# Performance work log

Hardware: AMD Instinct MI355X
Metric: run time of the kernel (lower is better)

## Reference

```python
import jax, jax.numpy as jnp
import numpy as np

N_HEADS = 16
EPS = 1e-5


def layer_norm(x, g, b):
    mu = jnp.mean(x, axis=-1, keepdims=True)
    var = jnp.mean(jnp.square(x - mu), axis=-1, keepdims=True)
    return (x - mu) * jax.lax.rsqrt(var + EPS) * g + b


def mhsa(X, wq, wk, wv, wfc, bfc):
    S, D = X.shape
    dk = D // N_HEADS
    scale = 1.0 / np.sqrt(dk).astype(np.float32)
    Q = (X @ wq).reshape(S, N_HEADS, dk).transpose(1, 0, 2)  # (H,S,dk)
    K = (X @ wk).reshape(S, N_HEADS, dk).transpose(1, 0, 2)
    V = (X @ wv).reshape(S, N_HEADS, dk).transpose(1, 0, 2)
    scores = jnp.einsum('hsd,htd->hst', Q, K) * scale
    attn = jax.nn.softmax(scores, axis=-1)
    ctx = jnp.einsum('hst,htd->hsd', attn, V)  # (H,S,dk)
    # Faithful to original torch code: transpose(1,2) on (H,S,dk) -> (H,dk,S),
    # then reshape(-1, H*dk). This scrambles features but is the module's math.
    ctx = jnp.transpose(ctx, (0, 2, 1)).reshape(-1, N_HEADS * dk)  # (S, H*dk)
    return ctx @ wfc + bfc


def setup_inputs() -> dict:
    key = jax.random.key(0)
    S, D = 2048, 2048
    ks = jax.random.split(key, 16)
    sd = 0.02
    p = lambda k, shp: jax.random.normal(k, shp, dtype=jnp.float32) * sd
    return {
        'X': jax.random.normal(ks[0], (S, D), dtype=jnp.float32),
        'wq1': p(ks[1], (D, D)), 'wk1': p(ks[2], (D, D)), 'wv1': p(ks[3], (D, D)),
        'wfc1': p(ks[4], (D, D)), 'bfc1': jnp.zeros((D,), jnp.float32),
        'g1': jnp.ones((D,), jnp.float32), 'b1': jnp.zeros((D,), jnp.float32),
        'wl1': p(ks[5], (D, D)), 'bl1': jnp.zeros((D,), jnp.float32),
        'g2': jnp.ones((D,), jnp.float32), 'b2': jnp.zeros((D,), jnp.float32),
        'wq2': p(ks[6], (D, D)), 'wk2': p(ks[7], (D, D)), 'wv2': p(ks[8], (D, D)),
        'wfc2': p(ks[9], (D, D)), 'bfc2': jnp.zeros((D,), jnp.float32),
        'g3': jnp.ones((D,), jnp.float32), 'b3': jnp.zeros((D,), jnp.float32),
        'wl2': p(ks[10], (D, D)), 'bl2': jnp.zeros((D,), jnp.float32),
        'g4': jnp.ones((D,), jnp.float32), 'b4': jnp.zeros((D,), jnp.float32),
    }


def reference(X, wq1, wk1, wv1, wfc1, bfc1, g1, b1, wl1, bl1, g2, b2,
              wq2, wk2, wv2, wfc2, bfc2, g3, b3, wl2, bl2, g4, b4):
    out = mhsa(X, wq1, wk1, wv1, wfc1, bfc1)
    X = layer_norm(out + X, g1, b1)
    out = X @ wl1 + bl1
    X = layer_norm(out + X, g2, b2)
    out = mhsa(X, wq2, wk2, wv2, wfc2, bfc2)
    X = layer_norm(out + X, g3, b3)
    out = X @ wl2 + bl2
    X = layer_norm(out + X, g4, b4)
    return X
```

## Files before the change

kernel.cpp:

```cpp
#include <hip/hip_runtime.h>
#include <stdint.h>

typedef __bf16 bf16_t;
typedef __bf16 bf16x8 __attribute__((ext_vector_type(8)));
typedef float  f32x4  __attribute__((ext_vector_type(4)));
typedef unsigned short u16x4 __attribute__((ext_vector_type(4)));

__device__ __forceinline__ void gl_lds16(const void* g, void* lds) {
  __builtin_amdgcn_global_load_lds(
      (const __attribute__((address_space(1))) uint32_t*)g,
      (__attribute__((address_space(3))) uint32_t*)lds, 16, 0, 0);
}

template<bool OUT_BF16, bool HAS_BIAS, bool HAS_RES>
__global__ __launch_bounds__(256)
void gemm_bt(const bf16_t* __restrict__ A, int64_t lda, int64_t sA,
             const bf16_t* __restrict__ BT, int64_t ldb, int64_t sB,
             void* __restrict__ Cv, int64_t ldc, int64_t sC,
             const float* __restrict__ bias, const float* __restrict__ res,
             float scale, int K)
{
  __shared__ __align__(16) bf16_t lA[128 * 32];
  __shared__ __align__(16) bf16_t lB[128 * 32];
  const int t = threadIdx.x;
  const int z = blockIdx.z;

  const int gx  = gridDim.x;
  const int nwg = gx * gridDim.y;
  int flat = blockIdx.y * gx + blockIdx.x;
  if ((nwg & 7) == 0) flat = (flat & 7) * (nwg >> 3) + (flat >> 3);
  const int tn = flat % gx;
  const int tm = flat / gx;

  const bf16_t* Ab = A + (int64_t)z * sA;
  const bf16_t* Bb = BT + (int64_t)z * sB;
  const int64_t bm = (int64_t)tm * 128;
  const int64_t bn = (int64_t)tn * 128;
  const int l   = t & 63;
  const int wid = t >> 6;
  const int wm  = (wid >> 1) * 64;
  const int wn  = (wid & 1) * 64;
  const int lr  = l & 15;
  const int kg  = l >> 4;
  const int srow = t >> 2;
  const int scol = (t & 3) * 8;
  char* lAc = (char*)lA;
  char* lBc = (char*)lB;
  const int wbase = (t & 192) * 16;

  f32x4 acc[4][4] = {};

  for (int k0 = 0; k0 < K; k0 += 32) {
    const bf16_t* ga = Ab + (bm + srow) * lda + k0 + scol;
    const bf16_t* gb = Bb + (bn + srow) * ldb + k0 + scol;
    gl_lds16(ga,            lAc + wbase);
    gl_lds16(ga + 64 * lda, lAc + 4096 + wbase);
    gl_lds16(gb,            lBc + wbase);
    gl_lds16(gb + 64 * ldb, lBc + 4096 + wbase);
    __syncthreads();
    bf16x8 af[4], bfv[4];
#pragma unroll
    for (int m = 0; m < 4; ++m)
      af[m] = *(const bf16x8*)(lA + (wm + m * 16 + lr) * 32 + kg * 8);
#pragma unroll
    for (int n = 0; n < 4; ++n)
      bfv[n] = *(const bf16x8*)(lB + (wn + n * 16 + lr) * 32 + kg * 8);
#pragma unroll
    for (int m = 0; m < 4; ++m)
#pragma unroll
      for (int n = 0; n < 4; ++n)
        acc[m][n] = __builtin_amdgcn_mfma_f32_16x16x32_bf16(af[m], bfv[n], acc[m][n], 0, 0, 0);
    __syncthreads();
  }

  bf16_t* C16 = (bf16_t*)Cv + (int64_t)z * sC;
  float*  C32 = (float*)Cv + (int64_t)z * sC;
#pragma unroll
  for (int m = 0; m < 4; ++m) {
#pragma unroll
    for (int n = 0; n < 4; ++n) {
      const int64_t col = bn + wn + n * 16 + lr;
      const float bv = HAS_BIAS ? bias[col] : 0.0f;
#pragma unroll
      for (int r = 0; r < 4; ++r) {
        const int64_t row = bm + wm + m * 16 + kg * 4 + r;
        float v = acc[m][n][r] * scale + bv;
        if constexpr (HAS_RES) v += res[row * ldc + col];
        if constexpr (OUT_BF16) C16[row * ldc + col] = (bf16_t)v;
        else                    C32[row * ldc + col] = v;
      }
    }
  }
}

__global__ __launch_bounds__(256)
void flash_attn(const bf16_t* __restrict__ QKV,
                const bf16_t* __restrict__ VT,
                bf16_t* __restrict__ CTXT)
{
  __shared__ __align__(16) bf16_t lK[64 * 128];
  __shared__ __align__(16) bf16_t lV[128 * 64];
  __shared__ __align__(16) bf16_t lP[4][16 * 64];
  const int t = threadIdx.x;
  const int w = t >> 6, l = t & 63, lo = l & 15, hi = l >> 4;
  const int head = blockIdx.y;
  const int qt = blockIdx.x;
  const int q0 = qt * 64 + w * 16;
  const int wbase = (t & 192) * 16;

  const bf16_t* qp = QKV + (int64_t)(q0 + lo) * 6144 + head * 128 + hi * 8;
  bf16x8 qf[4];
#pragma unroll
  for (int kk = 0; kk < 4; ++kk) qf[kk] = *(const bf16x8*)(qp + 32 * kk);

  const bf16_t* kbase = QKV + 2048 + head * 128;
  const bf16_t* vbase = VT + (int64_t)(head * 128) * 2048;

  float m_r[4], l_r[4];
  f32x4 Oacc[8] = {};
#pragma unroll
  for (int r = 0; r < 4; ++r) { m_r[r] = -3.0e38f; l_r[r] = 0.f; }

  const float c1 = 0.08838834764831845f * 1.4426950408889634f;

  char* lKc = (char*)lK;
  char* lVc = (char*)lV;
  char* pw  = (char*)lP[w];

  for (int tile = 0; tile < 32; ++tile) {
    const int kv0 = tile * 64;
#pragma unroll
    for (int c = 0; c < 4; ++c) {
      const int row = c * 16 + (t >> 4);
      const int srcb = ((t & 15) * 16) ^ ((row & 7) << 4);
      gl_lds16(kbase + (int64_t)(kv0 + row) * 6144 + (srcb >> 1), lKc + c * 4096 + wbase);
    }
#pragma unroll
    for (int c = 0; c < 4; ++c) {
      const int row = c * 32 + (t >> 3);
      const int srcb = ((t & 7) * 16) ^ ((row & 7) << 4);
      gl_lds16(vbase + (int64_t)row * 2048 + kv0 + (srcb >> 1), lVc + c * 4096 + wbase);
    }
    __syncthreads();

    f32x4 Sacc[4] = {};
#pragma unroll
    for (int kk = 0; kk < 4; ++kk) {
      bf16x8 kb[4];
#pragma unroll
      for (int n = 0; n < 4; ++n) {
        const int row = n * 16 + lo;
        kb[n] = *(const bf16x8*)(lKc + row * 256 + ((kk * 64 + hi * 16) ^ ((row & 7) << 4)));
      }
#pragma unroll
      for (int n = 0; n < 4; ++n)
        Sacc[n] = __builtin_amdgcn_mfma_f32_16x16x32_bf16(qf[kk], kb[n], Sacc[n], 0, 0, 0);
    }

    float corr[4];
#pragma unroll
    for (int r = 0; r < 4; ++r) {
      float mx = Sacc[0][r];
#pragma unroll
      for (int n = 1; n < 4; ++n) mx = fmaxf(mx, Sacc[n][r]);
#pragma unroll
      for (int off = 1; off < 16; off <<= 1) mx = fmaxf(mx, __shfl_xor(mx, off));
      const float mt = mx * c1;
      const float mnew = fmaxf(m_r[r], mt);
      corr[r] = exp2f(m_r[r] - mnew);
      m_r[r] = mnew;
    }
    float psum[4] = {0.f, 0.f, 0.f, 0.f};
#pragma unroll
    for (int n = 0; n < 4; ++n) {
#pragma unroll
      for (int r = 0; r < 4; ++r) {
        const float p = exp2f(Sacc[n][r] * c1 - m_r[r]);
        psum[r] += p;
        const int row = hi * 4 + r;
        const int byte = row * 128 + (((n * 16 + lo) * 2) ^ ((row & 7) << 4));
        *(bf16_t*)(pw + byte) = (bf16_t)p;
      }
    }
#pragma unroll
    for (int r = 0; r < 4; ++r) {
#pragma unroll
      for (int off = 1; off < 16; off <<= 1) psum[r] += __shfl_xor(psum[r], off);
      l_r[r] = l_r[r] * corr[r] + psum[r];
    }
#pragma unroll
    for (int n = 0; n < 8; ++n) {
      Oacc[n][0] *= corr[0]; Oacc[n][1] *= corr[1];
      Oacc[n][2] *= corr[2]; Oacc[n][3] *= corr[3];
    }
    asm volatile("s_waitcnt lgkmcnt(0)" ::: "memory");
    __builtin_amdgcn_sched_barrier(0);

#pragma unroll
    for (int kk = 0; kk < 2; ++kk) {
      const bf16x8 pa = *(const bf16x8*)(pw + lo * 128 + ((kk * 64 + hi * 16) ^ ((lo & 7) << 4)));
#pragma unroll
      for (int n = 0; n < 8; ++n) {
        const int row = n * 16 + lo;
        const bf16x8 vb = *(const bf16x8*)(lVc + row * 128 + ((kk * 64 + hi * 16) ^ ((row & 7) << 4)));
        Oacc[n] = __builtin_amdgcn_mfma_f32_16x16x32_bf16(pa, vb, Oacc[n], 0, 0, 0);
      }
    }
    __syncthreads();
  }

  float inv[4];
#pragma unroll
  for (int r = 0; r < 4; ++r) inv[r] = 1.0f / l_r[r];
#pragma unroll
  for (int n = 0; n < 8; ++n) {
    u16x4 o;
#pragma unroll
    for (int r = 0; r < 4; ++r) {
      const bf16_t b = (bf16_t)(Oacc[n][r] * inv[r]);
      o[r] = *(const unsigned short*)&b;
    }
    *(u16x4*)(CTXT + (int64_t)(head * 128 + n * 16 + lo) * 2048 + q0 + hi * 4) = o;
  }
}

template<typename TIN>
__device__ __forceinline__
void transpose_body(const TIN* __restrict__ in, int64_t ldi,
                    bf16_t* __restrict__ out, int64_t ldo)
{
  __shared__ float tile[32][33];
  const int bx = blockIdx.x * 32;
  const int by = blockIdx.y * 32;
  const int tx = threadIdx.x & 31;
  const int ty = threadIdx.x >> 5;
#pragma unroll
  for (int i = 0; i < 32; i += 8)
    tile[ty + i][tx] = (float)in[(int64_t)(by + ty + i) * ldi + bx + tx];
  __syncthreads();
#pragma unroll
  for (int i = 0; i < 32; i += 8)
    out[(int64_t)(bx + ty + i) * ldo + by + tx] = (bf16_t)tile[tx][ty + i];
}

template<typename TIN>
__global__ __launch_bounds__(256)
void transpose_to_bf16(const TIN* __restrict__ in, int64_t ldi,
                       bf16_t* __restrict__ out, int64_t ldo)
{
  transpose_body<TIN>(in, ldi, out, ldo);
}

struct Ptr10 { const float* p[10]; };

__global__ __launch_bounds__(256)
void weight_prep(Ptr10 ws, bf16_t* __restrict__ out, int64_t stride)
{
  transpose_body<float>(ws.p[blockIdx.z], 2048, out + (int64_t)blockIdx.z * stride, 2048);
}

__global__ __launch_bounds__(256)
void f32_to_bf16_k(const float* __restrict__ in, bf16_t* __restrict__ out)
{
  const int64_t i = ((int64_t)blockIdx.x * 256 + threadIdx.x) * 8;
  const float4 a = *(const float4*)(in + i);
  const float4 b = *(const float4*)(in + i + 4);
  bf16x8 o;
  o[0] = (bf16_t)a.x; o[1] = (bf16_t)a.y; o[2] = (bf16_t)a.z; o[3] = (bf16_t)a.w;
  o[4] = (bf16_t)b.x; o[5] = (bf16_t)b.y; o[6] = (bf16_t)b.z; o[7] = (bf16_t)b.w;
  *(bf16x8*)(out + i) = o;
}

__global__ __launch_bounds__(256)
void add_ln(const float* __restrict__ y,
            const float* __restrict__ g, const float* __restrict__ b,
            float* __restrict__ xout, bf16_t* __restrict__ xb)
{
  const int64_t row = blockIdx.x;
  const int t = threadIdx.x;
  const int64_t base = row * 2048 + t * 8;
  const float4 y0 = *(const float4*)(y + base);
  const float4 y1 = *(const float4*)(y + base + 4);
  float x[8] = {y0.x, y0.y, y0.z, y0.w, y1.x, y1.y, y1.z, y1.w};
  float s = 0.f, q = 0.f;
#pragma unroll
  for (int j = 0; j < 8; ++j) { s += x[j]; q += x[j] * x[j]; }
#pragma unroll
  for (int off = 32; off; off >>= 1) { s += __shfl_xor(s, off); q += __shfl_xor(q, off); }
  __shared__ float rs[4], rq[4];
  const int l = t & 63, w = t >> 6;
  if (l == 0) { rs[w] = s; rq[w] = q; }
  __syncthreads();
  s = rs[0] + rs[1] + rs[2] + rs[3];
  q = rq[0] + rq[1] + rq[2] + rq[3];
  const float mean = s * (1.f / 2048.f);
  const float var  = q * (1.f / 2048.f) - mean * mean;
  const float inv  = rsqrtf(var + 1e-5f);
  const float4 g0 = *(const float4*)(g + t * 8);
  const float4 g1 = *(const float4*)(g + t * 8 + 4);
  const float4 b0 = *(const float4*)(b + t * 8);
  const float4 b1 = *(const float4*)(b + t * 8 + 4);
  float o[8];
  o[0] = (x[0] - mean) * inv * g0.x + b0.x; o[1] = (x[1] - mean) * inv * g0.y + b0.y;
  o[2] = (x[2] - mean) * inv * g0.z + b0.z; o[3] = (x[3] - mean) * inv * g0.w + b0.w;
  o[4] = (x[4] - mean) * inv * g1.x + b1.x; o[5] = (x[5] - mean) * inv * g1.y + b1.y;
  o[6] = (x[6] - mean) * inv * g1.z + b1.z; o[7] = (x[7] - mean) * inv * g1.w + b1.w;
  *(float4*)(xout + base)     = make_float4(o[0], o[1], o[2], o[3]);
  *(float4*)(xout + base + 4) = make_float4(o[4], o[5], o[6], o[7]);
  bf16x8 ob;
#pragma unroll
  for (int j = 0; j < 8; ++j) ob[j] = (bf16_t)o[j];
  *(bf16x8*)(xb + base) = ob;
}

extern "C" void kernel_launch(void* const* d_in, const int* in_sizes, int n_in,
                              void* d_out, int out_size, void* d_ws, size_t ws_size,
                              hipStream_t stream)
{
  constexpr int S = 2048, D = 2048;
  constexpr int64_t DD = (int64_t)D * D;

  const float* X    = (const float*)d_in[0];
  const float* wq1  = (const float*)d_in[1];
  const float* wk1  = (const float*)d_in[2];
  const float* wv1  = (const float*)d_in[3];
  const float* wfc1 = (const float*)d_in[4];
  const float* bfc1 = (const float*)d_in[5];
  const float* g1   = (const float*)d_in[6];
  const float* b1   = (const float*)d_in[7];
  const float* wl1  = (const float*)d_in[8];
  const float* bl1  = (const float*)d_in[9];
  const float* g2   = (const float*)d_in[10];
  const float* b2   = (const float*)d_in[11];
  const float* wq2  = (const float*)d_in[12];
  const float* wk2  = (const float*)d_in[13];
  const float* wv2  = (const float*)d_in[14];
  const float* wfc2 = (const float*)d_in[15];
  const float* bfc2 = (const float*)d_in[16];
  const float* g3   = (const float*)d_in[17];
  const float* b3   = (const float*)d_in[18];
  const float* wl2  = (const float*)d_in[19];
  const float* bl2  = (const float*)d_in[20];
  const float* g4   = (const float*)d_in[21];
  const float* b4   = (const float*)d_in[22];

  char* p = (char*)d_ws;
  bf16_t* WT  = (bf16_t*)p; p += 10 * DD * 2;
  bf16_t* Xb  = (bf16_t*)p; p += DD * 2;
  bf16_t* QKV = (bf16_t*)p; p += (int64_t)S * 3 * D * 2;
  bf16_t* VT  = (bf16_t*)p; p += DD * 2;
  bf16_t* CTXT= (bf16_t*)p; p += DD * 2;
  float*  OUTF= (float*)p;  p += DD * 4;
  float*  XF  = (float*)p;

  const dim3 TB(256);

  auto gemm = [&](const bf16_t* A, int64_t lda,
                  const bf16_t* BT, int64_t ldb,
                  void* C, int64_t ldc,
                  const float* bias, const float* res, float scale,
                  int M, int N, int K, bool obf) {
    dim3 gg(N / 128, M / 128, 1);
    if (obf) gemm_bt<true, false, false><<<gg, TB, 0, stream>>>(A, lda, 0, BT, ldb, 0, C, ldc, 0, nullptr, nullptr, scale, K);
    else     gemm_bt<false, true, true ><<<gg, TB, 0, stream>>>(A, lda, 0, BT, ldb, 0, C, ldc, 0, bias, res, scale, K);
  };

  Ptr10 wsrc = {{wq1, wk1, wv1, wfc1, wl1, wq2, wk2, wv2, wfc2, wl2}};
  weight_prep<<<dim3(64, 64, 10), TB, 0, stream>>>(wsrc, WT, DD);
  f32_to_bf16_k<<<dim3(DD / 2048), TB, 0, stream>>>(X, Xb);

  auto layer = [&](const float* resX, int sq, int sfc, int sfl,
                   const float* bfc, const float* ga, const float* ba,
                   const float* bl, const float* gb, const float* bb,
                   float* ln2_out) {
    gemm(Xb, D, WT + (int64_t)sq * DD, D, QKV, 3 * D, nullptr, nullptr, 1.f, S, 3 * D, D, true);
    transpose_to_bf16<bf16_t><<<dim3(64, 64), TB, 0, stream>>>(QKV + 2 * D, 3 * D, VT, S);
    flash_attn<<<dim3(32, 16), TB, 0, stream>>>(QKV, VT, CTXT);
    gemm(CTXT, S, WT + (int64_t)sfc * DD, D, OUTF, D, bfc, resX, 1.f, D, D, S, false);
    add_ln<<<dim3(S), TB, 0, stream>>>(OUTF, ga, ba, XF, Xb);
    gemm(Xb, D, WT + (int64_t)sfl * DD, D, OUTF, D, bl, XF, 1.f, S, D, D, false);
    add_ln<<<dim3(S), TB, 0, stream>>>(OUTF, gb, bb, ln2_out, Xb);
  };

  layer(X,  0, 3, 4, bfc1, g1, b1, bl1, g2, b2, XF);
  layer(XF, 5, 8, 9, bfc2, g3, b3, bl2, g4, b4, (float*)d_out);
}
```

Before: 849.4 us.

## Split attention KV and square GEMMs into two partitions with merge kernels

Flash attention now runs with a split-KV grid of two halves, each writing fp32 partial outputs plus row max and sum, and a new merge kernel combines them into the bf16 context. The two square 2048x2048 GEMMs become split-K launches over two halves writing fp32 partials. Bias and residual are now added inside an extended add+layernorm kernel that sums both partials. This doubles the grid to fill more CUs (the originals launched only 512 and 256 blocks), at the cost of extra fp32 partial traffic and one more kernel per attention.

```diff
diff --git a/kernel.cpp b/kernel.cpp
--- a/kernel.cpp
+++ b/kernel.cpp
@@ -4,7 +4,6 @@
 typedef __bf16 bf16_t;
 typedef __bf16 bf16x8 __attribute__((ext_vector_type(8)));
 typedef float  f32x4  __attribute__((ext_vector_type(4)));
-typedef unsigned short u16x4 __attribute__((ext_vector_type(4)));
 
 __device__ __forceinline__ void gl_lds16(const void* g, void* lds) {
   __builtin_amdgcn_global_load_lds(
@@ -96,7 +95,9 @@
 __global__ __launch_bounds__(256)
 void flash_attn(const bf16_t* __restrict__ QKV,
                 const bf16_t* __restrict__ VT,
-                bf16_t* __restrict__ CTXT)
+                float* __restrict__ Opart,
+                float* __restrict__ Mb,
+                float* __restrict__ Lb)
 {
   __shared__ __align__(16) bf16_t lK[64 * 128];
   __shared__ __align__(16) bf16_t lV[128 * 64];
@@ -105,6 +106,7 @@
   const int w = t >> 6, l = t & 63, lo = l & 15, hi = l >> 4;
   const int head = blockIdx.y;
   const int qt = blockIdx.x;
+  const int z = blockIdx.z;
   const int q0 = qt * 64 + w * 16;
   const int wbase = (t & 192) * 16;
 
@@ -127,8 +129,8 @@
   char* lVc = (char*)lV;
   char* pw  = (char*)lP[w];
 
-  for (int tile = 0; tile < 32; ++tile) {
-    const int kv0 = tile * 64;
+  for (int tile = 0; tile < 16; ++tile) {
+    const int kv0 = z * 1024 + tile * 64;
 #pragma unroll
     for (int c = 0; c < 4; ++c) {
       const int row = c * 16 + (t >> 4);
@@ -212,16 +214,56 @@
   float inv[4];
 #pragma unroll
   for (int r = 0; r < 4; ++r) inv[r] = 1.0f / l_r[r];
+  float* op = Opart + (int64_t)z * 2048 * 2048 + (int64_t)(head * 128) * 2048;
 #pragma unroll
   for (int n = 0; n < 8; ++n) {
-    u16x4 o;
-#pragma unroll
-    for (int r = 0; r < 4; ++r) {
-      const bf16_t b = (bf16_t)(Oacc[n][r] * inv[r]);
-      o[r] = *(const unsigned short*)&b;
-    }
-    *(u16x4*)(CTXT + (int64_t)(head * 128 + n * 16 + lo) * 2048 + q0 + hi * 4) = o;
-  }
+    f32x4 o = {Oacc[n][0] * inv[0], Oacc[n][1] * inv[1],
+               Oacc[n][2] * inv[2], Oacc[n][3] * inv[3]};
+    *(f32x4*)(op + (int64_t)(n * 16 + lo) * 2048 + q0 + hi * 4) = o;
+  }
+  if (lo == 0) {
+    const int mlb = (z * 16 + head) * 2048 + q0 + hi * 4;
+#pragma unroll
+    for (int r = 0; r < 4; ++r) { Mb[mlb + r] = m_r[r]; Lb[mlb + r] = l_r[r]; }
+  }
+}
+
+__global__ __launch_bounds__(256)
+void merge_attn(const float* __restrict__ Opart, const float* __restrict__ Mb,
+                const float* __restrict__ Lb, bf16_t* __restrict__ CTXT)
+{
+  const int row = blockIdx.x;
+  const int head = row >> 7;
+  const int q = threadIdx.x * 8;
+  const int64_t DD = 2048LL * 2048;
+  const float* o0 = Opart + (int64_t)row * 2048;
+  const float* o1 = o0 + DD;
+  const float* m0p = Mb + head * 2048;
+  const float* m1p = m0p + 16 * 2048;
+  const float* l0p = Lb + head * 2048;
+  const float* l1p = l0p + 16 * 2048;
+  bf16x8 out;
+#pragma unroll
+  for (int h = 0; h < 2; ++h) {
+    const int qq = q + h * 4;
+    const float4 a  = *(const float4*)(o0 + qq);
+    const float4 c  = *(const float4*)(o1 + qq);
+    const float4 m0 = *(const float4*)(m0p + qq);
+    const float4 m1 = *(const float4*)(m1p + qq);
+    const float4 l0 = *(const float4*)(l0p + qq);
+    const float4 l1 = *(const float4*)(l1p + qq);
+    const float oa[4] = {a.x, a.y, a.z, a.w}, oc[4] = {c.x, c.y, c.z, c.w};
+    const float ma[4] = {m0.x, m0.y, m0.z, m0.w}, mc[4] = {m1.x, m1.y, m1.z, m1.w};
+    const float la[4] = {l0.x, l0.y, l0.z, l0.w}, lc[4] = {l1.x, l1.y, l1.z, l1.w};
+#pragma unroll
+    for (int j = 0; j < 4; ++j) {
+      const float m  = fmaxf(ma[j], mc[j]);
+      const float w0 = la[j] * exp2f(ma[j] - m);
+      const float w1 = lc[j] * exp2f(mc[j] - m);
+      out[h * 4 + j] = (bf16_t)((w0 * oa[j] + w1 * oc[j]) / (w0 + w1));
+    }
+  }
+  *(bf16x8*)(CTXT + (int64_t)row * 2048 + q) = out;
 }
 
 template<typename TIN>
@@ -272,16 +314,26 @@
 }
 
 __global__ __launch_bounds__(256)
-void add_ln(const float* __restrict__ y,
-            const float* __restrict__ g, const float* __restrict__ b,
-            float* __restrict__ xout, bf16_t* __restrict__ xb)
+void add_ln2(const float* __restrict__ y0, const float* __restrict__ y1,
+             const float* __restrict__ res, const float* __restrict__ bias,
+             const float* __restrict__ g, const float* __restrict__ b,
+             float* __restrict__ xout, bf16_t* __restrict__ xb)
 {
   const int64_t row = blockIdx.x;
   const int t = threadIdx.x;
   const int64_t base = row * 2048 + t * 8;
-  const float4 y0 = *(const float4*)(y + base);
-  const float4 y1 = *(const float4*)(y + base + 4);
-  float x[8] = {y0.x, y0.y, y0.z, y0.w, y1.x, y1.y, y1.z, y1.w};
+  const float4 a0 = *(const float4*)(y0 + base);
+  const float4 a1 = *(const float4*)(y0 + base + 4);
+  const float4 c0 = *(const float4*)(y1 + base);
+  const float4 c1 = *(const float4*)(y1 + base + 4);
+  const float4 r0 = *(const float4*)(res + base);
+  const float4 r1 = *(const float4*)(res + base + 4);
+  const float4 e0 = *(const float4*)(bias + t * 8);
+  const float4 e1 = *(const float4*)(bias + t * 8 + 4);
+  float x[8] = {a0.x + c0.x + r0.x + e0.x, a0.y + c0.y + r0.y + e0.y,
+                a0.z + c0.z + r0.z + e0.z, a0.w + c0.w + r0.w + e0.w,
+                a1.x + c1.x + r1.x + e1.x, a1.y + c1.y + r1.y + e1.y,
+                a1.z + c1.z + r1.z + e1.z, a1.w + c1.w + r1.w + e1.w};
   float s = 0.f, q = 0.f;
 #pragma unroll
   for (int j = 0; j < 8; ++j) { s += x[j]; q += x[j] * x[j]; }
@@ -345,24 +397,31 @@
   const float* b4   = (const float*)d_in[22];
 
   char* p = (char*)d_ws;
-  bf16_t* WT  = (bf16_t*)p; p += 10 * DD * 2;
-  bf16_t* Xb  = (bf16_t*)p; p += DD * 2;
-  bf16_t* QKV = (bf16_t*)p; p += (int64_t)S * 3 * D * 2;
-  bf16_t* VT  = (bf16_t*)p; p += DD * 2;
-  bf16_t* CTXT= (bf16_t*)p; p += DD * 2;
-  float*  OUTF= (float*)p;  p += DD * 4;
-  float*  XF  = (float*)p;
+  bf16_t* WT   = (bf16_t*)p; p += 10 * DD * 2;
+  bf16_t* Xb   = (bf16_t*)p; p += DD * 2;
+  bf16_t* QKV  = (bf16_t*)p; p += (int64_t)S * 3 * D * 2;
+  bf16_t* VT   = (bf16_t*)p; p += DD * 2;
+  bf16_t* CTXT = (bf16_t*)p; p += DD * 2;
+  float*  OUTF = (float*)p;  p += 2 * DD * 4;
+  float*  XF   = (float*)p;  p += DD * 4;
+  float*  OP   = (float*)p;  p += 2 * DD * 4;
+  float*  Mb   = (float*)p;  p += 2 * 16 * 2048 * 4;
+  float*  Lb   = (float*)p;
 
   const dim3 TB(256);
 
-  auto gemm = [&](const bf16_t* A, int64_t lda,
-                  const bf16_t* BT, int64_t ldb,
-                  void* C, int64_t ldc,
-                  const float* bias, const float* res, float scale,
-                  int M, int N, int K, bool obf) {
+  auto gemm_full = [&](const bf16_t* A, int64_t lda,
+                       const bf16_t* BT, int64_t ldb,
+                       void* C, int64_t ldc, int M, int N, int K) {
     dim3 gg(N / 128, M / 128, 1);
-    if (obf) gemm_bt<true, false, false><<<gg, TB, 0, stream>>>(A, lda, 0, BT, ldb, 0, C, ldc, 0, nullptr, nullptr, scale, K);
-    else     gemm_bt<false, true, true ><<<gg, TB, 0, stream>>>(A, lda, 0, BT, ldb, 0, C, ldc, 0, bias, res, scale, K);
+    gemm_bt<true, false, false><<<gg, TB, 0, stream>>>(A, lda, 0, BT, ldb, 0, C, ldc, 0,
+                                                       nullptr, nullptr, 1.f, K);
+  };
+  auto gemm_splitk = [&](const bf16_t* A, int64_t lda,
+                         const bf16_t* BT, int64_t ldb, float* C) {
+    dim3 gg(16, 16, 2);
+    gemm_bt<false, false, false><<<gg, TB, 0, stream>>>(A, lda, 1024, BT, ldb, 1024,
+                                                        C, D, DD, nullptr, nullptr, 1.f, 1024);
   };
 
   Ptr10 wsrc = {{wq1, wk1, wv1, wfc1, wl1, wq2, wk2, wv2, wfc2, wl2}};
@@ -373,13 +432,14 @@
                    const float* bfc, const float* ga, const float* ba,
                    const float* bl, const float* gb, const float* bb,
                    float* ln2_out) {
-    gemm(Xb, D, WT + (int64_t)sq * DD, D, QKV, 3 * D, nullptr, nullptr, 1.f, S, 3 * D, D, true);
+    gemm_full(Xb, D, WT + (int64_t)sq * DD, D, QKV, 3 * D, S, 3 * D, D);
     transpose_to_bf16<bf16_t><<<dim3(64, 64), TB, 0, stream>>>(QKV + 2 * D, 3 * D, VT, S);
-    flash_attn<<<dim3(32, 16), TB, 0, stream>>>(QKV, VT, CTXT);
-    gemm(CTXT, S, WT + (int64_t)sfc * DD, D, OUTF, D, bfc, resX, 1.f, D, D, S, false);
-    add_ln<<<dim3(S), TB, 0, stream>>>(OUTF, ga, ba, XF, Xb);
-    gemm(Xb, D, WT + (int64_t)sfl * DD, D, OUTF, D, bl, XF, 1.f, S, D, D, false);
-    add_ln<<<dim3(S), TB, 0, stream>>>(OUTF, gb, bb, ln2_out, Xb);
+    flash_attn<<<dim3(32, 16, 2), TB, 0, stream>>>(QKV, VT, OP, Mb, Lb);
+    merge_attn<<<dim3(2048), TB, 0, stream>>>(OP, Mb, Lb, CTXT);
+    gemm_splitk(CTXT, S, WT + (int64_t)sfc * DD, D, OUTF);
+    add_ln2<<<dim3(S), TB, 0, stream>>>(OUTF, OUTF + DD, resX, bfc, ga, ba, XF, Xb);
+    gemm_splitk(Xb, D, WT + (int64_t)sfl * DD, D, OUTF);
+    add_ln2<<<dim3(S), TB, 0, stream>>>(OUTF, OUTF + DD, XF, bl, gb, bb, ln2_out, Xb);
   };
 
   layer(X,  0, 3, 4, bfc1, g1, b1, bl1, g2, b2, XF);
```

Result: faster. 805.9 us (-5.1%).
